# Performance work log

Measured on AMD Instinct MI355X. Metric: run time of the kernel, lower is better.

The kernel has to match this reference:

```python
import jax, jax.numpy as jnp
import numpy as np

B, S, D = 4, 512, 2048      # batch, seq, hidden
DFF = 5632                   # SwiGLU intermediate
E, TOPK, R = 8, 2, 16        # experts, top-k, lora rank
SCALE = 32.0 / 16.0          # lora alpha / r


def setup_inputs() -> dict:
    key = jax.random.key(0)
    ks = jax.random.split(key, 18)
    rn = lambda k, shape, s=0.02: (jax.random.normal(k, shape, dtype=jnp.float32) * s)
    return {
        "data": jax.random.normal(ks[0], (B, S, D), dtype=jnp.float32),
        # shared base SwiGLU MLP (gate/up/down projections)
        "W1": rn(ks[1], (DFF, D)),
        "W3": rn(ks[2], (DFF, D)),
        "W2": rn(ks[3], (D, DFF)),
        # MixLoRA MoE adapter: router gate + per-expert LoRA on w1/w3/w2
        "gate_W": rn(ks[4], (E, D)),
        "A1": rn(ks[5], (E, R, D)), "B1": rn(ks[6], (E, DFF, R)),
        "A3": rn(ks[7], (E, R, D)), "B3": rn(ks[8], (E, DFF, R)),
        "A2": rn(ks[9], (E, R, DFF)), "B2": rn(ks[10], (E, D, R)),
        # plain LoRA adapter (second batch segment, _lora_forward path)
        "la1": rn(ks[11], (R, D)), "lb1": rn(ks[12], (DFF, R)),
        "la3": rn(ks[13], (R, D)), "lb3": rn(ks[14], (DFF, R)),
        "la2": rn(ks[15], (R, DFF)), "lb2": rn(ks[16], (D, R)),
    }


def reference(data, W1, W3, W2, gate_W, A1, B1, A3, B3, A2, B2,
              la1, lb1, la3, lb3, la2, lb2):
    half = B // 2

    # ---- segment 0: MixLoRA MoE adapter ----
    x = data[:half].reshape(-1, D)                      # [N, D] tokens
    N = x.shape[0]
    logits = x @ gate_W.T                               # [N, E] router logits
    probs = jax.nn.softmax(logits, axis=-1)
    topw, topi = jax.lax.top_k(probs, TOPK)
    topw = topw / jnp.sum(topw, axis=-1, keepdims=True)
    # dense routing weights (zero for non-selected experts)
    wd = jnp.zeros((N, E), x.dtype).at[jnp.arange(N)[:, None], topi].set(topw)

    bg = x @ W1.T                                       # [N, DFF] base gate proj
    bu = x @ W3.T                                       # [N, DFF] base up proj
    dg = jnp.einsum('enr,efr->enf', jnp.einsum('nd,erd->enr', x, A1), B1)
    du = jnp.einsum('enr,efr->enf', jnp.einsum('nd,erd->enr', x, A3), B3)
    h = jax.nn.silu(bg[None] + SCALE * dg) * (bu[None] + SCALE * du)  # [E,N,DFF]
    oe = jnp.einsum('enf,df->end', h, W2) \
        + SCALE * jnp.einsum('enr,edr->end', jnp.einsum('enf,erf->enr', h, A2), B2)
    moe_out = jnp.einsum('ne,end->nd', wd, oe).reshape(half, S, D)

    # ---- segment 1: plain LoRA adapter (_lora_forward) ----
    x2 = data[half:]                                    # [half, S, D]
    g2 = jax.nn.silu(x2 @ W1.T + SCALE * ((x2 @ la1.T) @ lb1.T))
    u2 = x2 @ W3.T + SCALE * ((x2 @ la3.T) @ lb3.T)
    h2 = g2 * u2
    out2 = h2 @ W2.T + SCALE * ((h2 @ la2.T) @ lb2.T)

    # index_copy over contiguous per-segment ranges == concat along dim 0
    final = jnp.concatenate([moe_out, out2], axis=0)    # [B, S, D]
    return final, logits
```

## Files before the change

kernel.cpp:

```cpp
#include <hip/hip_runtime.h>
#include <hip/hip_bf16.h>

#define DEVI __device__ __forceinline__

typedef __attribute__((ext_vector_type(8))) short short8;
typedef __attribute__((ext_vector_type(4))) float f32x4;
typedef unsigned short ushort_t;

constexpr int D    = 2048;
constexpr int DFF  = 5632;
constexpr int NTOK = 2048;
constexpr int NMOE = 1024;
constexpr float KSCALE = 2.0f;

constexpr int NW      = 11776;
constexpr int COL_A1  = 11264;
constexpr int COL_A3  = 11392;
constexpr int COL_LA1 = 11520;
constexpr int COL_LA3 = 11536;

DEVI float bf2f(unsigned short u) { return __uint_as_float(((unsigned)u) << 16); }
DEVI unsigned short f2bf(float f) {
  unsigned u = __float_as_uint(f);
  u += 0x7FFFu + ((u >> 16) & 1u);
  return (unsigned short)(u >> 16);
}
DEVI float silu(float x) { return x / (1.f + __expf(-x)); }

template <int V> struct IC { static constexpr int value = V; };

struct CastSegs {
  const float* src[14];
  unsigned short* dst[14];
  int blk_end[14];
};

__global__ __launch_bounds__(256) void cast_segs_kernel(CastSegs cs) {
  int b = blockIdx.x;
  int s = 0;
  #pragma unroll
  for (int i = 0; i < 14; ++i) if (b >= cs.blk_end[i]) s = i + 1;
  int bstart = (s == 0) ? 0 : cs.blk_end[s - 1];
  size_t idx = ((size_t)(b - bstart) * 256 + threadIdx.x) * 4;
  float4 v = *(const float4*)(cs.src[s] + idx);
  ushort4 o;
  o.x = f2bf(v.x); o.y = f2bf(v.y); o.z = f2bf(v.z); o.w = f2bf(v.w);
  *(ushort4*)(cs.dst[s] + idx) = o;
}

__global__ __launch_bounds__(256) void transpose_ra_kernel(const float* __restrict__ A2,
                                                           const float* __restrict__ la2,
                                                           unsigned short* __restrict__ A2tb,
                                                           unsigned short* __restrict__ la2tb) {
  int f = blockIdx.x * 256 + threadIdx.x;
  int e = blockIdx.y;
  const float* src = (e < 8) ? (A2 + (size_t)e * 16 * DFF) : la2;
  unsigned short* dst = (e < 8) ? (A2tb + (size_t)e * DFF * 16) : la2tb;
  unsigned short tmp[16];
  #pragma unroll
  for (int r = 0; r < 16; ++r) tmp[r] = f2bf(src[(size_t)r * DFF + f]);
  #pragma unroll
  for (int r = 0; r < 16; ++r) dst[(size_t)f * 16 + r] = tmp[r];
}

__global__ __launch_bounds__(256) void gate_kernel(const float* __restrict__ x,
                                                   const float* __restrict__ gW,
                                                   float* __restrict__ logits_out,
                                                   int* __restrict__ gidx,
                                                   float* __restrict__ gwt) {
  int t = blockIdx.x * 4 + (threadIdx.x >> 6);
  int lane = threadIdx.x & 63;
  const float* xr = x + (size_t)t * D;
  float acc[8];
  #pragma unroll
  for (int e = 0; e < 8; ++e) acc[e] = 0.f;
  for (int k = lane; k < D; k += 64) {
    float xv = xr[k];
    #pragma unroll
    for (int e = 0; e < 8; ++e) acc[e] = fmaf(xv, gW[e * D + k], acc[e]);
  }
  #pragma unroll
  for (int e = 0; e < 8; ++e) {
    float v = acc[e];
    #pragma unroll
    for (int s = 32; s > 0; s >>= 1) v += __shfl_xor(v, s);
    acc[e] = v;
  }
  if (lane == 0) {
    #pragma unroll
    for (int e = 0; e < 8; ++e) logits_out[(size_t)t * 8 + e] = acc[e];
    int i1 = 0;
    #pragma unroll
    for (int e = 1; e < 8; ++e) if (acc[e] > acc[i1]) i1 = e;
    int i2 = (i1 == 0) ? 1 : 0;
    #pragma unroll
    for (int e = 0; e < 8; ++e) if (e != i1 && acc[e] > acc[i2]) i2 = e;
    float w1 = 1.f / (1.f + expf(acc[i2] - acc[i1]));
    gidx[t * 2] = i1; gidx[t * 2 + 1] = i2;
    gwt[t * 2] = w1;  gwt[t * 2 + 1] = 1.f - w1;
  }
}

typedef const void __attribute__((address_space(1)))* gp1_t;
typedef void __attribute__((address_space(3)))* lp3_t;
DEVI void gload_lds16(const void* g, void* l) {
  __builtin_amdgcn_global_load_lds((gp1_t)g, (lp3_t)l, 16, 0, 0);
}
#define S_BARRIER() asm volatile("s_barrier" ::: "memory")

template <int BM, int BN, int WM, int WN, int EPI>
__global__ __launch_bounds__(WM * WN * 64, 2) void gemm8(
    const unsigned short* __restrict__ A,
    const unsigned short* __restrict__ B,
    int K,
    float* __restrict__ Cf,
    unsigned short* __restrict__ Cb,
    const float* __restrict__ addv,
    int ldc, int nbx) {
  constexpr int THREADS = WM * WN * 64;
  constexpr int RW = BM / WM;
  constexpr int CW = BN / WN;
  constexpr int FM = RW / 16;
  constexpr int FN = CW / 16;
  constexpr int FM2 = FM / 2, FN2 = FN / 2;
  constexpr int TILEB = BM * 128;

  __shared__ __align__(16) char smem[4 * TILEB];

  const int tid = threadIdx.x;
  const int wave = tid >> 6, lane = tid & 63;
  const int wm = wave / WN, wn = wave % WN;
  const int r15 = lane & 15, g = lane >> 4;

  const int nwg = (int)gridDim.x;
  const int bid = (int)blockIdx.x;
  const int wgid = (bid & 7) * (nwg >> 3) + (bid >> 3);
  const int bx = wgid % nbx, by = wgid / nbx;

  const unsigned short* Ablk = A + (size_t)by * BM * K;
  const unsigned short* Bblk = B + (size_t)bx * BN * K;

  int sgo[4];
  #pragma unroll
  for (int j = 0; j < 4; ++j) {
    int tt = j * THREADS + tid;
    int row = tt >> 3;
    int col = (((tt & 7) ^ (row & 7)) << 3);
    sgo[j] = row * K + col;
  }
  auto stage = [&](const unsigned short* blk, int k0, char* bufdst) {
    #pragma unroll
    for (int j = 0; j < 4; ++j)
      gload_lds16((const char*)blk + ((size_t)(sgo[j] + k0) << 1),
                  bufdst + j * (THREADS * 16) + wave * 1024);
  };

  const int aldb = (wm * RW + r15) * 128;
  const int bldb = (wn * CW + r15) * 128;
  const int sl0 = ((g ^ (r15 & 7)) << 4);
  const int sl1 = (((4 + g) ^ (r15 & 7)) << 4);

  f32x4 acc[FM][FN];
  #pragma unroll
  for (int m = 0; m < FM; ++m)
    #pragma unroll
    for (int n = 0; n < FN; ++n)
      #pragma unroll
      for (int j = 0; j < 4; ++j) acc[m][n][j] = 0.f;

  int cur = 0;
  const int NT = K >> 6;

  auto phase = [&](auto QMC, auto QNC, bool stB, int k0s) {
    constexpr int QM = decltype(QMC)::value;
    constexpr int QN = decltype(QNC)::value;
    const char* bA = smem + cur * (2 * TILEB);
    const char* bB = bA + TILEB;
    short8 af[FM2][2], bq[FN2][2];
    #pragma unroll
    for (int i = 0; i < FM2; ++i) {
      af[i][0] = *(const short8*)(bA + aldb + (QM * (RW / 2) + i * 16) * 128 + sl0);
      af[i][1] = *(const short8*)(bA + aldb + (QM * (RW / 2) + i * 16) * 128 + sl1);
    }
    #pragma unroll
    for (int n = 0; n < FN2; ++n) {
      bq[n][0] = *(const short8*)(bB + bldb + (QN * (CW / 2) + n * 16) * 128 + sl0);
      bq[n][1] = *(const short8*)(bB + bldb + (QN * (CW / 2) + n * 16) * 128 + sl1);
    }
    if (stB) stage(Bblk, k0s, smem + (cur ^ 1) * (2 * TILEB) + TILEB);
    S_BARRIER();
    __builtin_amdgcn_s_setprio(1);
    #pragma unroll
    for (int i = 0; i < FM2; ++i)
      #pragma unroll
      for (int n = 0; n < FN2; ++n)
        #pragma unroll
        for (int kk = 0; kk < 2; ++kk)
          acc[QM * FM2 + i][QN * FN2 + n] = __builtin_amdgcn_mfma_f32_16x16x32_bf16(
              af[i][kk], bq[n][kk], acc[QM * FM2 + i][QN * FN2 + n], 0, 0, 0);
    __builtin_amdgcn_s_setprio(0);
    S_BARRIER();
  };

  stage(Ablk, 0, smem);
  stage(Bblk, 0, smem + TILEB);

  for (int t = 0; t < NT; ++t, cur ^= 1) {
    const bool hn = (t + 1) < NT;
    const int k0n = (t + 1) << 6;
    if (hn) {
      stage(Ablk, k0n, smem + (cur ^ 1) * (2 * TILEB));
      asm volatile("s_waitcnt vmcnt(4)" ::: "memory");
    } else {
      asm volatile("s_waitcnt vmcnt(0)" ::: "memory");
    }
    S_BARRIER();
    phase(IC<0>{}, IC<0>{}, false, 0);
    phase(IC<0>{}, IC<1>{}, hn, k0n);
    phase(IC<1>{}, IC<0>{}, false, 0);
    phase(IC<1>{}, IC<1>{}, false, 0);
  }

  const int row0 = by * BM + wm * RW + (g << 2);
  const int col0 = bx * BN + wn * CW + r15;
  #pragma unroll
  for (int m = 0; m < FM; ++m) {
    #pragma unroll
    for (int n = 0; n < FN; ++n) {
      int col = col0 + n * 16;
      #pragma unroll
      for (int j = 0; j < 4; ++j) {
        int row = row0 + m * 16 + j;
        size_t off = (size_t)row * ldc + col;
        float v = acc[m][n][j];
        if (EPI == 1) Cb[off] = f2bf(v);
        else          Cf[off] = v + addv[off];
      }
    }
  }
}

DEVI float dot16bf(const float* a, const unsigned short* w) {
  short8 w0 = *(const short8*)w;
  short8 w1 = *(const short8*)(w + 8);
  float s = 0.f;
  #pragma unroll
  for (int i = 0; i < 8; ++i) s = fmaf(a[i],     bf2f((unsigned short)w0[i]), s);
  #pragma unroll
  for (int i = 0; i < 8; ++i) s = fmaf(a[8 + i], bf2f((unsigned short)w1[i]), s);
  return s;
}

__global__ __launch_bounds__(256) void h_kernel(
    const unsigned short* __restrict__ GU,
    const unsigned short* __restrict__ B1b,
    const unsigned short* __restrict__ B3b,
    const unsigned short* __restrict__ A2tb,
    const unsigned short* __restrict__ lb1b,
    const unsigned short* __restrict__ lb3b,
    const unsigned short* __restrict__ la2tb,
    const int* __restrict__ gidx, const float* __restrict__ gwt,
    unsigned short* __restrict__ Hb,
    float* __restrict__ qw) {
  const int t = blockIdx.x;
  const int tid = threadIdx.x;
  const unsigned short* gu = GU + (size_t)t * NW;
  unsigned short* hrow = Hb + (size_t)t * DFF;
  float qacc[32];
  #pragma unroll
  for (int r = 0; r < 32; ++r) qacc[r] = 0.f;
  float w1 = 0.f, w2 = 0.f;

  if (t < NMOE) {
    const int e1 = gidx[t * 2], e2 = gidx[t * 2 + 1];
    w1 = gwt[t * 2]; w2 = gwt[t * 2 + 1];
    float xa1a[16], xa1b[16], xa3a[16], xa3b[16];
    #pragma unroll
    for (int r = 0; r < 16; ++r) {
      xa1a[r] = bf2f(gu[COL_A1 + e1 * 16 + r]);
      xa1b[r] = bf2f(gu[COL_A1 + e2 * 16 + r]);
      xa3a[r] = bf2f(gu[COL_A3 + e1 * 16 + r]);
      xa3b[r] = bf2f(gu[COL_A3 + e2 * 16 + r]);
    }
    const unsigned short* B1e1 = B1b + (size_t)e1 * DFF * 16;
    const unsigned short* B1e2 = B1b + (size_t)e2 * DFF * 16;
    const unsigned short* B3e1 = B3b + (size_t)e1 * DFF * 16;
    const unsigned short* B3e2 = B3b + (size_t)e2 * DFF * 16;
    const unsigned short* A2e1 = A2tb + (size_t)e1 * DFF * 16;
    const unsigned short* A2e2 = A2tb + (size_t)e2 * DFF * 16;
    for (int i = 0; i < 22; ++i) {
      int f = tid + i * 256;
      float bg = bf2f(gu[f]), bu = bf2f(gu[DFF + f]);
      float dg1 = dot16bf(xa1a, B1e1 + f * 16);
      float du1 = dot16bf(xa3a, B3e1 + f * 16);
      float dg2 = dot16bf(xa1b, B1e2 + f * 16);
      float du2 = dot16bf(xa3b, B3e2 + f * 16);
      float h1 = silu(bg + KSCALE * dg1) * (bu + KSCALE * du1);
      float h2 = silu(bg + KSCALE * dg2) * (bu + KSCALE * du2);
      hrow[f] = f2bf(w1 * h1 + w2 * h2);
      short8 a0 = *(const short8*)(A2e1 + f * 16);
      short8 a1 = *(const short8*)(A2e1 + f * 16 + 8);
      short8 b0 = *(const short8*)(A2e2 + f * 16);
      short8 b1 = *(const short8*)(A2e2 + f * 16 + 8);
      #pragma unroll
      for (int r = 0; r < 8; ++r) {
        qacc[r]      = fmaf(h1, bf2f((unsigned short)a0[r]), qacc[r]);
        qacc[8 + r]  = fmaf(h1, bf2f((unsigned short)a1[r]), qacc[8 + r]);
        qacc[16 + r] = fmaf(h2, bf2f((unsigned short)b0[r]), qacc[16 + r]);
        qacc[24 + r] = fmaf(h2, bf2f((unsigned short)b1[r]), qacc[24 + r]);
      }
    }
  } else {
    float s1[16], s3[16];
    #pragma unroll
    for (int r = 0; r < 16; ++r) {
      s1[r] = bf2f(gu[COL_LA1 + r]);
      s3[r] = bf2f(gu[COL_LA3 + r]);
    }
    for (int i = 0; i < 22; ++i) {
      int f = tid + i * 256;
      float bg = bf2f(gu[f]), bu = bf2f(gu[DFF + f]);
      float dg = dot16bf(s1, lb1b + f * 16);
      float du = dot16bf(s3, lb3b + f * 16);
      float h = silu(bg + KSCALE * dg) * (bu + KSCALE * du);
      hrow[f] = f2bf(h);
      short8 a0 = *(const short8*)(la2tb + f * 16);
      short8 a1 = *(const short8*)(la2tb + f * 16 + 8);
      #pragma unroll
      for (int r = 0; r < 8; ++r) {
        qacc[r]     = fmaf(h, bf2f((unsigned short)a0[r]), qacc[r]);
        qacc[8 + r] = fmaf(h, bf2f((unsigned short)a1[r]), qacc[8 + r]);
      }
    }
  }

  #pragma unroll
  for (int r = 0; r < 32; ++r) {
    float v = qacc[r];
    #pragma unroll
    for (int s = 32; s > 0; s >>= 1) v += __shfl_xor(v, s);
    qacc[r] = v;
  }
  __shared__ float red[4][32];
  const int wave = tid >> 6, lane = tid & 63;
  if (lane == 0) {
    #pragma unroll
    for (int r = 0; r < 32; ++r) red[wave][r] = qacc[r];
  }
  __syncthreads();
  if (tid < 32) {
    float v = red[0][tid] + red[1][tid] + red[2][tid] + red[3][tid];
    float sc = (t < NMOE) ? ((tid < 16) ? (KSCALE * w1) : (KSCALE * w2)) : KSCALE;
    qw[(size_t)t * 32 + tid] = v * sc;
  }
}

__global__ __launch_bounds__(256) void ylora_kernel(const float* __restrict__ qw,
                                                    const unsigned short* __restrict__ B2b,
                                                    const unsigned short* __restrict__ lb2b,
                                                    const int* __restrict__ gidx,
                                                    float* __restrict__ ylora) {
  const int t = blockIdx.x;
  const int tid = threadIdx.x;
  const float* qr = qw + (size_t)t * 32;
  float q1[16], q2[16];
  #pragma unroll
  for (int r = 0; r < 16; ++r) { q1[r] = qr[r]; q2[r] = qr[16 + r]; }
  if (t < NMOE) {
    const unsigned short* p1 = B2b + (size_t)gidx[t * 2] * D * 16;
    const unsigned short* p2 = B2b + (size_t)gidx[t * 2 + 1] * D * 16;
    #pragma unroll
    for (int i = 0; i < 8; ++i) {
      int d = tid + i * 256;
      ylora[(size_t)t * D + d] = dot16bf(q1, p1 + d * 16) + dot16bf(q2, p2 + d * 16);
    }
  } else {
    #pragma unroll
    for (int i = 0; i < 8; ++i) {
      int d = tid + i * 256;
      ylora[(size_t)t * D + d] = dot16bf(q1, lb2b + d * 16);
    }
  }
}

extern "C" void kernel_launch(void* const* d_in, const int* in_sizes, int n_in,
                              void* d_out, int out_size, void* d_ws, size_t ws_size,
                              hipStream_t stream) {
  (void)in_sizes; (void)n_in; (void)out_size; (void)ws_size;
  const float* data = (const float*)d_in[0];
  const float* W1   = (const float*)d_in[1];
  const float* W3   = (const float*)d_in[2];
  const float* W2   = (const float*)d_in[3];
  const float* gW   = (const float*)d_in[4];
  const float* A1   = (const float*)d_in[5];
  const float* B1   = (const float*)d_in[6];
  const float* A3   = (const float*)d_in[7];
  const float* B3   = (const float*)d_in[8];
  const float* A2   = (const float*)d_in[9];
  const float* B2   = (const float*)d_in[10];
  const float* la1  = (const float*)d_in[11];
  const float* lb1  = (const float*)d_in[12];
  const float* la3  = (const float*)d_in[13];
  const float* lb3  = (const float*)d_in[14];
  const float* la2  = (const float*)d_in[15];
  const float* lb2  = (const float*)d_in[16];

  char* w = (char*)d_ws;
  size_t off = 0;
  auto alloc = [&](size_t bytes) -> char* {
    char* p = w + off;
    off += (bytes + 255) & ~(size_t)255;
    return p;
  };
  unsigned short* xb    = (unsigned short*)alloc((size_t)NTOK * D * 2);
  unsigned short* W13b  = (unsigned short*)alloc((size_t)NW * D * 2);
  unsigned short* W2b   = (unsigned short*)alloc((size_t)D * DFF * 2);
  unsigned short* B1b   = (unsigned short*)alloc((size_t)8 * DFF * 16 * 2);
  unsigned short* B3b   = (unsigned short*)alloc((size_t)8 * DFF * 16 * 2);
  unsigned short* A2tb  = (unsigned short*)alloc((size_t)8 * DFF * 16 * 2);
  unsigned short* la2tb = (unsigned short*)alloc((size_t)DFF * 16 * 2);
  unsigned short* lb1b  = (unsigned short*)alloc((size_t)DFF * 16 * 2);
  unsigned short* lb3b  = (unsigned short*)alloc((size_t)DFF * 16 * 2);
  unsigned short* lb2b  = (unsigned short*)alloc((size_t)D * 16 * 2);
  unsigned short* B2b   = (unsigned short*)alloc((size_t)8 * D * 16 * 2);
  int*   gidx = (int*)alloc((size_t)NMOE * 2 * 4);
  float* gwt  = (float*)alloc((size_t)NMOE * 2 * 4);
  unsigned short* GU    = (unsigned short*)alloc((size_t)NTOK * NW * 2);

  unsigned short* Hb = W13b;
  float* ylora = (float*)((char*)W13b + (size_t)NTOK * DFF * 2);
  float* qw    = (float*)xb;

  CastSegs cs;
  const float* srcs[14] = {data, W1, W3, W2, A1, A3, la1, la3, B1, B3, lb1, lb3, lb2, B2};
  unsigned short* dsts[14] = {
      xb, W13b, W13b + (size_t)DFF * D, W2b,
      W13b + (size_t)COL_A1 * D, W13b + (size_t)COL_A3 * D,
      W13b + (size_t)COL_LA1 * D, W13b + (size_t)COL_LA3 * D,
      B1b, B3b, lb1b, lb3b, lb2b, B2b};
  int ns[14] = {NTOK * D, DFF * D, DFF * D, DFF * D, 128 * D, 128 * D, 16 * D, 16 * D,
                8 * DFF * 16, 8 * DFF * 16, DFF * 16, DFF * 16, D * 16, 8 * D * 16};
  int total_blocks = 0;
  for (int i = 0; i < 14; ++i) {
    cs.src[i] = srcs[i];
    cs.dst[i] = dsts[i];
    total_blocks += ns[i] / 1024;
    cs.blk_end[i] = total_blocks;
  }
  cast_segs_kernel<<<total_blocks, 256, 0, stream>>>(cs);
  transpose_ra_kernel<<<dim3(DFF / 256, 9), 256, 0, stream>>>(A2, la2, A2tb, la2tb);
  hipMemsetAsync(W13b + (size_t)11552 * D, 0, (size_t)(NW - 11552) * D * 2, stream);

  gate_kernel<<<NMOE / 4, 256, 0, stream>>>(data, gW,
      (float*)d_out + (size_t)NTOK * D, gidx, gwt);

  gemm8<256, 256, 2, 4, 1><<<(NW / 256) * (NTOK / 256), 512, 0, stream>>>(
      xb, W13b, D, (float*)nullptr, GU, (const float*)nullptr, NW, NW / 256);

  h_kernel<<<NTOK, 256, 0, stream>>>(GU, B1b, B3b, A2tb, lb1b, lb3b, la2tb,
                                     gidx, gwt, Hb, qw);

  ylora_kernel<<<NTOK, 256, 0, stream>>>(qw, B2b, lb2b, gidx, ylora);

  gemm8<128, 128, 2, 2, 2><<<(D / 128) * (NTOK / 128), 256, 0, stream>>>(
      Hb, W2b, DFF, (float*)d_out, (unsigned short*)nullptr, ylora, D, D / 128);
}
```

Measured before the change: 386.0 us.

## Generalize GEMM to multi-buffer pipeline with rectangular tiles and trim padded width

Replaces the fixed double-buffered gemm8 with a templated gemmT that supports separate A/B tile heights, an N-deep LDS ring (triple buffering for the gate/up GEMM) and configurable phase splitting. B fragments are loaded once per k-step and reused across A phases. The fused W1/W3/LoRA projection width shrinks from 11776 to 11648 columns, which cuts padded work, and it uses 256x128 tiles. The down-projection GEMM moves from 4 to 8 waves per block with a higher occupancy hint. The cost is more LDS use per block, higher register pressure, and possible occupancy limits.

Result: faster. 360.6 us (-6.6%).

```diff
diff --git a/kernel.cpp b/kernel.cpp
--- a/kernel.cpp
+++ b/kernel.cpp
@@ -5,7 +5,6 @@
 
 typedef __attribute__((ext_vector_type(8))) short short8;
 typedef __attribute__((ext_vector_type(4))) float f32x4;
-typedef unsigned short ushort_t;
 
 constexpr int D    = 2048;
 constexpr int DFF  = 5632;
@@ -13,7 +12,7 @@
 constexpr int NMOE = 1024;
 constexpr float KSCALE = 2.0f;
 
-constexpr int NW      = 11776;
+constexpr int NW      = 11648;
 constexpr int COL_A1  = 11264;
 constexpr int COL_A3  = 11392;
 constexpr int COL_LA1 = 11520;
@@ -26,8 +25,6 @@
   return (unsigned short)(u >> 16);
 }
 DEVI float silu(float x) { return x / (1.f + __expf(-x)); }
-
-template <int V> struct IC { static constexpr int value = V; };
 
 struct CastSegs {
   const float* src[14];
@@ -108,8 +105,17 @@
 }
 #define S_BARRIER() asm volatile("s_barrier" ::: "memory")
 
-template <int BM, int BN, int WM, int WN, int EPI>
-__global__ __launch_bounds__(WM * WN * 64, 2) void gemm8(
+template <int N> DEVI void vmcnt_() {
+  static_assert(N == 0 || N == 4 || N == 6 || N == 8 || N == 12, "enumerate literals");
+  if constexpr (N == 0)  asm volatile("s_waitcnt vmcnt(0)" ::: "memory");
+  if constexpr (N == 4)  asm volatile("s_waitcnt vmcnt(4)" ::: "memory");
+  if constexpr (N == 6)  asm volatile("s_waitcnt vmcnt(6)" ::: "memory");
+  if constexpr (N == 8)  asm volatile("s_waitcnt vmcnt(8)" ::: "memory");
+  if constexpr (N == 12) asm volatile("s_waitcnt vmcnt(12)" ::: "memory");
+}
+
+template <int BM, int BN, int WM, int WN, int NBUF, int NPH, int MINW, int EPI>
+__global__ __launch_bounds__(WM * WN * 64, MINW) void gemmT(
     const unsigned short* __restrict__ A,
     const unsigned short* __restrict__ B,
     int K,
@@ -120,12 +126,17 @@
   constexpr int THREADS = WM * WN * 64;
   constexpr int RW = BM / WM;
   constexpr int CW = BN / WN;
-  constexpr int FM = RW / 16;
-  constexpr int FN = CW / 16;
-  constexpr int FM2 = FM / 2, FN2 = FN / 2;
-  constexpr int TILEB = BM * 128;
-
-  __shared__ __align__(16) char smem[4 * TILEB];
+  constexpr int FM = RW / 16, FN = CW / 16;
+  constexpr int FMP = FM / NPH;
+  constexpr int ATILE = BM * 128;
+  constexpr int BTILE = BN * 128;
+  constexpr int SLOT = ATILE + BTILE;
+  constexpr int APARTS = BM * 8 / THREADS;
+  constexpr int BPARTS = BN * 8 / THREADS;
+  constexpr int LOADS = APARTS + BPARTS;
+  constexpr int PD = NBUF - 1;
+
+  __shared__ __align__(16) char smem[NBUF * SLOT];
 
   const int tid = threadIdx.x;
   const int wave = tid >> 6, lane = tid & 63;
@@ -140,25 +151,35 @@
   const unsigned short* Ablk = A + (size_t)by * BM * K;
   const unsigned short* Bblk = B + (size_t)bx * BN * K;
 
-  int sgo[4];
-  #pragma unroll
-  for (int j = 0; j < 4; ++j) {
+  int sgoA[APARTS], sgoB[BPARTS];
+  #pragma unroll
+  for (int j = 0; j < APARTS; ++j) {
     int tt = j * THREADS + tid;
     int row = tt >> 3;
-    int col = (((tt & 7) ^ (row & 7)) << 3);
-    sgo[j] = row * K + col;
-  }
-  auto stage = [&](const unsigned short* blk, int k0, char* bufdst) {
-    #pragma unroll
-    for (int j = 0; j < 4; ++j)
-      gload_lds16((const char*)blk + ((size_t)(sgo[j] + k0) << 1),
-                  bufdst + j * (THREADS * 16) + wave * 1024);
+    sgoA[j] = row * K + (((tt & 7) ^ (row & 7)) << 3);
+  }
+  #pragma unroll
+  for (int j = 0; j < BPARTS; ++j) {
+    int tt = j * THREADS + tid;
+    int row = tt >> 3;
+    sgoB[j] = row * K + (((tt & 7) ^ (row & 7)) << 3);
+  }
+  auto stage = [&](int slot, int k0) {
+    char* s = smem + slot * SLOT;
+    #pragma unroll
+    for (int j = 0; j < APARTS; ++j)
+      gload_lds16((const char*)Ablk + ((size_t)(sgoA[j] + k0) << 1),
+                  s + j * (THREADS * 16) + wave * 1024);
+    #pragma unroll
+    for (int j = 0; j < BPARTS; ++j)
+      gload_lds16((const char*)Bblk + ((size_t)(sgoB[j] + k0) << 1),
+                  s + ATILE + j * (THREADS * 16) + wave * 1024);
   };
 
-  const int aldb = (wm * RW + r15) * 128;
-  const int bldb = (wn * CW + r15) * 128;
-  const int sl0 = ((g ^ (r15 & 7)) << 4);
-  const int sl1 = (((4 + g) ^ (r15 & 7)) << 4);
+  const int arow0 = (wm * RW + r15) * 128;
+  const int brow0 = (wn * CW + r15) * 128;
+  const int s0 = ((g ^ (r15 & 7)) << 4);
+  const int s1 = (((4 + g) ^ (r15 & 7)) << 4);
 
   f32x4 acc[FM][FN];
   #pragma unroll
@@ -168,57 +189,54 @@
       #pragma unroll
       for (int j = 0; j < 4; ++j) acc[m][n][j] = 0.f;
 
-  int cur = 0;
   const int NT = K >> 6;
 
-  auto phase = [&](auto QMC, auto QNC, bool stB, int k0s) {
-    constexpr int QM = decltype(QMC)::value;
-    constexpr int QN = decltype(QNC)::value;
-    const char* bA = smem + cur * (2 * TILEB);
-    const char* bB = bA + TILEB;
-    short8 af[FM2][2], bq[FN2][2];
-    #pragma unroll
-    for (int i = 0; i < FM2; ++i) {
-      af[i][0] = *(const short8*)(bA + aldb + (QM * (RW / 2) + i * 16) * 128 + sl0);
-      af[i][1] = *(const short8*)(bA + aldb + (QM * (RW / 2) + i * 16) * 128 + sl1);
-    }
-    #pragma unroll
-    for (int n = 0; n < FN2; ++n) {
-      bq[n][0] = *(const short8*)(bB + bldb + (QN * (CW / 2) + n * 16) * 128 + sl0);
-      bq[n][1] = *(const short8*)(bB + bldb + (QN * (CW / 2) + n * 16) * 128 + sl1);
-    }
-    if (stB) stage(Bblk, k0s, smem + (cur ^ 1) * (2 * TILEB) + TILEB);
+  #pragma unroll
+  for (int d = 0; d < PD; ++d) stage(d, d << 6);
+
+  int slCur = 0, slAhead = PD % NBUF;
+  for (int t = 0; t < NT; ++t) {
+    if (t + PD < NT) {
+      stage(slAhead, (t + PD) << 6);
+      vmcnt_<PD * LOADS>();
+    } else if (PD == 2 && t + 1 < NT) {
+      vmcnt_<LOADS>();
+    } else {
+      vmcnt_<0>();
+    }
     S_BARRIER();
-    __builtin_amdgcn_s_setprio(1);
-    #pragma unroll
-    for (int i = 0; i < FM2; ++i)
-      #pragma unroll
-      for (int n = 0; n < FN2; ++n)
+
+    const char* sA = smem + slCur * SLOT;
+    const char* sB = sA + ATILE;
+    short8 bq[FN][2];
+    #pragma unroll
+    for (int n = 0; n < FN; ++n) {
+      bq[n][0] = *(const short8*)(sB + brow0 + n * 16 * 128 + s0);
+      bq[n][1] = *(const short8*)(sB + brow0 + n * 16 * 128 + s1);
+    }
+    #pragma unroll
+    for (int p = 0; p < NPH; ++p) {
+      short8 af[FMP][2];
+      #pragma unroll
+      for (int i = 0; i < FMP; ++i) {
+        int ro = arow0 + (p * FMP + i) * 16 * 128;
+        af[i][0] = *(const short8*)(sA + ro + s0);
+        af[i][1] = *(const short8*)(sA + ro + s1);
+      }
+      __builtin_amdgcn_s_setprio(1);
+      #pragma unroll
+      for (int i = 0; i < FMP; ++i)
         #pragma unroll
-        for (int kk = 0; kk < 2; ++kk)
-          acc[QM * FM2 + i][QN * FN2 + n] = __builtin_amdgcn_mfma_f32_16x16x32_bf16(
-              af[i][kk], bq[n][kk], acc[QM * FM2 + i][QN * FN2 + n], 0, 0, 0);
-    __builtin_amdgcn_s_setprio(0);
+        for (int n = 0; n < FN; ++n)
+          #pragma unroll
+          for (int kk = 0; kk < 2; ++kk)
+            acc[p * FMP + i][n] = __builtin_amdgcn_mfma_f32_16x16x32_bf16(
+                af[i][kk], bq[n][kk], acc[p * FMP + i][n], 0, 0, 0);
+      __builtin_amdgcn_s_setprio(0);
+    }
     S_BARRIER();
-  };
-
-  stage(Ablk, 0, smem);
-  stage(Bblk, 0, smem + TILEB);
-
-  for (int t = 0; t < NT; ++t, cur ^= 1) {
-    const bool hn = (t + 1) < NT;
-    const int k0n = (t + 1) << 6;
-    if (hn) {
-      stage(Ablk, k0n, smem + (cur ^ 1) * (2 * TILEB));
-      asm volatile("s_waitcnt vmcnt(4)" ::: "memory");
-    } else {
-      asm volatile("s_waitcnt vmcnt(0)" ::: "memory");
-    }
-    S_BARRIER();
-    phase(IC<0>{}, IC<0>{}, false, 0);
-    phase(IC<0>{}, IC<1>{}, hn, k0n);
-    phase(IC<1>{}, IC<0>{}, false, 0);
-    phase(IC<1>{}, IC<1>{}, false, 0);
+    slCur = (slCur + 1 == NBUF) ? 0 : slCur + 1;
+    slAhead = (slAhead + 1 == NBUF) ? 0 : slAhead + 1;
   }
 
   const int row0 = by * BM + wm * RW + (g << 2);
@@ -454,14 +472,14 @@
   gate_kernel<<<NMOE / 4, 256, 0, stream>>>(data, gW,
       (float*)d_out + (size_t)NTOK * D, gidx, gwt);
 
-  gemm8<256, 256, 2, 4, 1><<<(NW / 256) * (NTOK / 256), 512, 0, stream>>>(
-      xb, W13b, D, (float*)nullptr, GU, (const float*)nullptr, NW, NW / 256);
+  gemmT<256, 128, 2, 4, 3, 2, 2, 1><<<(NTOK / 256) * (NW / 128), 512, 0, stream>>>(
+      xb, W13b, D, (float*)nullptr, GU, (const float*)nullptr, NW, NW / 128);
 
   h_kernel<<<NTOK, 256, 0, stream>>>(GU, B1b, B3b, A2tb, lb1b, lb3b, la2tb,
                                      gidx, gwt, Hb, qw);
 
   ylora_kernel<<<NTOK, 256, 0, stream>>>(qw, B2b, lb2b, gidx, ylora);
 
-  gemm8<128, 128, 2, 2, 2><<<(D / 128) * (NTOK / 128), 256, 0, stream>>>(
+  gemmT<128, 128, 2, 4, 2, 2, 4, 2><<<(NTOK / 128) * (D / 128), 512, 0, stream>>>(
       Hb, W2b, DFF, (float*)d_out, (unsigned short*)nullptr, ylora, D, D / 128);
 }
```
